# Optimization experiments

Measured on AMD Instinct MI355X. Metric: run time of the kernel, lower is better.

The kernel has to match this reference:

```python
import jax, jax.numpy as jnp
import numpy as np

NUM_HEADS = 16
HEAD_DIM = 64


def setup_inputs() -> dict:
    key = jax.random.key(0)
    ks = jax.random.split(key, 6)
    B, S, E = 4, 1024, 1024
    return {
        "x": jax.random.normal(ks[0], (B, S, E), dtype=jnp.float32),
        "W_qkv": jax.random.normal(ks[1], (E, 3 * E), dtype=jnp.float32) * 0.02,
        "b_qkv": jax.random.normal(ks[2], (3 * E,), dtype=jnp.float32) * 0.02,
        "pe": jax.random.normal(ks[3], (S, S, HEAD_DIM), dtype=jnp.float32) * 0.02,
        "W_out": jax.random.normal(ks[4], (E, E), dtype=jnp.float32) * 0.02,
        "b_out": jax.random.normal(ks[5], (E,), dtype=jnp.float32) * 0.02,
    }


def reference(x, W_qkv, b_qkv, pe, W_out, b_out):
    B, S, E = x.shape
    H, D = NUM_HEADS, HEAD_DIM
    scale = D ** -0.5
    # qkv projection: (B,S,3E) -> (3,B,H,S,D)
    qkv = (x @ W_qkv + b_qkv).reshape(B, S, 3, H, D).transpose(2, 0, 3, 1, 4)
    q, k, v = qkv[0], qkv[1], qkv[2]
    # raw scaled scores (NO softmax in original module)
    scores = jnp.einsum('bhxd,bhyd->bhxy', q, k) * scale
    # relative position bias: pe is (S,S,D) == (x,y,c); original permutes to (c,x,y)
    # then einsum('cxy,bnxc->bnxy', pe, q) -> equivalent to 'xyc,bhxc->bhxy'
    pe_q = jnp.einsum('xyc,bhxc->bhxy', pe, q) * scale
    attn = (scores + pe_q) @ v                      # (B,H,S,D)
    out = attn.transpose(0, 2, 1, 3).reshape(B, S, E)
    return out @ W_out + b_out
```

## Files before the change

kernel.cpp:

```cpp
#include <hip/hip_runtime.h>
#include <cstdint>
#include <cstddef>


typedef unsigned short u16;
typedef unsigned char  u8;
typedef __bf16 bf16x8 __attribute__((ext_vector_type(8)));
typedef float  f32x4  __attribute__((ext_vector_type(4)));
typedef unsigned short u16x8 __attribute__((ext_vector_type(8)));

#define MFMA16(a, b, c) __builtin_amdgcn_mfma_f32_16x16x32_bf16((a), (b), (c), 0, 0, 0)

#define GLOAD16(g, l)                                                        \
    __builtin_amdgcn_global_load_lds(                                        \
        (const __attribute__((address_space(1))) unsigned int*)(g),          \
        (__attribute__((address_space(3))) unsigned int*)(l), 16, 0, 0)

__device__ __forceinline__ u16 f2bf(float f) {
    __bf16 h = (__bf16)f;
    return __builtin_bit_cast(u16, h);
}
__device__ __forceinline__ u16x8 pack8(float4 a, float4 b) {
    u16x8 v;
    v[0] = f2bf(a.x); v[1] = f2bf(a.y); v[2] = f2bf(a.z); v[3] = f2bf(a.w);
    v[4] = f2bf(b.x); v[5] = f2bf(b.y); v[6] = f2bf(b.z); v[7] = f2bf(b.w);
    return v;
}

__device__ __forceinline__ void sbar() {
    asm volatile("" ::: "memory");
    __builtin_amdgcn_s_barrier();
    asm volatile("" ::: "memory");
}
template <int N> __device__ __forceinline__ void waitv() {
    asm volatile("s_waitcnt vmcnt(%0)" :: "n"(N) : "memory");
}

__device__ __forceinline__ void convT_tile(const float* __restrict__ in,
                                           u16* __restrict__ out, int R, int C,
                                           int bx, int by, float (*tile)[68]) {
    const int t  = threadIdx.x;
    const int r0 = by * 64, c0 = bx * 64;
    const int rr = t >> 4, c4 = t & 15;
    for (int p = 0; p < 4; ++p) {
        int r = rr + p * 16;
        float4 v = *(const float4*)&in[(size_t)(r0 + r) * C + c0 + c4 * 4];
        *(float4*)&tile[r][c4 * 4] = v;
    }
    __syncthreads();
    for (int p = 0; p < 4; ++p) {
        int n = rr + p * 16;
        ushort4 o;
        o.x = f2bf(tile[c4 * 4 + 0][n]);
        o.y = f2bf(tile[c4 * 4 + 1][n]);
        o.z = f2bf(tile[c4 * 4 + 2][n]);
        o.w = f2bf(tile[c4 * 4 + 3][n]);
        *(ushort4*)&out[(size_t)(c0 + n) * R + r0 + c4 * 4] = o;
    }
}

__global__ __launch_bounds__(256) void kprep(const float* __restrict__ x,
                                             u16* __restrict__ xb,
                                             const float* __restrict__ Wqkv,
                                             u16* __restrict__ wqkvT,
                                             const float* __restrict__ Wout,
                                             u16* __restrict__ woutT) {
    __shared__ float tile[64][68];
    const int bid = blockIdx.x;
    if (bid < 2048) {
        int i = (bid * 256 + threadIdx.x) * 8;
        float4 f0 = *(const float4*)&x[i];
        float4 f1 = *(const float4*)&x[i + 4];
        *(u16x8*)&xb[i] = pack8(f0, f1);
    } else if (bid < 2816) {
        int r = bid - 2048;
        convT_tile(Wqkv, wqkvT, 1024, 3072, r % 48, r / 48, tile);
    } else {
        int r = bid - 2816;
        convT_tile(Wout, woutT, 1024, 1024, r % 16, r / 16, tile);
    }
}

__global__ __launch_bounds__(256, 2) void kgemm_qkv(const u16* __restrict__ A,
                                                    const u16* __restrict__ WT,
                                                    const float* __restrict__ bias,
                                                    u16* __restrict__ qb,
                                                    u16* __restrict__ kb,
                                                    u16* __restrict__ vtb) {
    __shared__ u16 a_s[128 * 64];
    __shared__ u16 b_s[128 * 64];
    const int t = threadIdx.x;
    const int m0 = blockIdx.y * 128, n0 = blockIdx.x * 128;
    const int lane = t & 63, w = t >> 6, lm = lane & 15, lq = lane >> 4;
    const int mb = (w >> 1) * 64, nb = (w & 1) * 64;
    const int sr = t >> 3, sc = (t & 7) * 8;

    f32x4 acc[4][4] = {};
    for (int k0 = 0; k0 < 1024; k0 += 64) {
        __syncthreads();
#pragma unroll
        for (int p = 0; p < 4; ++p) {
            GLOAD16(&A [(size_t)(m0 + p * 32 + sr) * 1024 + k0 + sc], &a_s[p * 2048 + t * 8]);
            GLOAD16(&WT[(size_t)(n0 + p * 32 + sr) * 1024 + k0 + sc], &b_s[p * 2048 + t * 8]);
        }
        __syncthreads();
#pragma unroll
        for (int ks = 0; ks < 2; ++ks) {
            bf16x8 af[4], bfr[4];
#pragma unroll
            for (int mt = 0; mt < 4; ++mt)
                af[mt] = *(const bf16x8*)&a_s[(mb + mt * 16 + lm) * 64 + ks * 32 + lq * 8];
#pragma unroll
            for (int nt = 0; nt < 4; ++nt)
                bfr[nt] = *(const bf16x8*)&b_s[(nb + nt * 16 + lm) * 64 + ks * 32 + lq * 8];
#pragma unroll
            for (int mt = 0; mt < 4; ++mt)
#pragma unroll
                for (int nt = 0; nt < 4; ++nt)
                    acc[mt][nt] = MFMA16(af[mt], bfr[nt], acc[mt][nt]);
        }
    }
    for (int nt = 0; nt < 4; ++nt) {
        int col = n0 + nb + nt * 16 + lm;
        float bv = bias[col];
        int which = col >> 10;
        int h = (col >> 6) & 15, d = col & 63;
        for (int mt = 0; mt < 4; ++mt) {
            int row0 = m0 + mb + mt * 16 + lq * 4;
            int b = row0 >> 10, s = row0 & 1023;
            if (which == 2) {
                ushort4 o;
                o.x = f2bf(acc[mt][nt][0] + bv);
                o.y = f2bf(acc[mt][nt][1] + bv);
                o.z = f2bf(acc[mt][nt][2] + bv);
                o.w = f2bf(acc[mt][nt][3] + bv);
                *(ushort4*)&vtb[((size_t)(b * 16 + h) * 64 + d) * 1024 + s] = o;
            } else {
                u16* dst = (which == 0) ? qb : kb;
                for (int i = 0; i < 4; ++i)
                    dst[((size_t)((b * 16 + h) * 1024 + s + i)) * 64 + d] =
                        f2bf(acc[mt][nt][i] + bv);
            }
        }
    }
}

__global__ __launch_bounds__(256, 4) void kpq(const u16* __restrict__ qb,
                                              const float* __restrict__ pe,
                                              u8* __restrict__ Pq) {
    __shared__ u16 q_s[64 * 64];
    __shared__ u16 pe_s[2][64 * 80];
    const int x = blockIdx.x;
    const int t = threadIdx.x;
    const int lane = t & 63, w = t >> 6, lm = lane & 15, lq = lane >> 4;
#pragma unroll
    for (int p = 0; p < 2; ++p)
        GLOAD16(&qb[(size_t)((p * 32 + (t >> 3)) * 1024 + x) * 64 + (t & 7) * 8],
                &q_s[p * 2048 + t * 8]);
    const int yl = t >> 2, cq = (t & 3) * 16;
    const float* pex = pe + (size_t)x * 65536;
    float4 r0, r1, r2, r3;
    {
        const float* src = &pex[(size_t)yl * 64 + cq];
        r0 = *(const float4*)&src[0];  r1 = *(const float4*)&src[4];
        r2 = *(const float4*)&src[8];  r3 = *(const float4*)&src[12];
    }
    u8* pq_base = Pq + ((size_t)lm * 1024 + x) * 1024 + lq * 16 + w * 4;
    int cur = 0;
    for (int it = 0; it < 16; ++it) {
        *(u16x8*)&pe_s[cur][yl * 80 + cq]     = pack8(r0, r1);
        *(u16x8*)&pe_s[cur][yl * 80 + cq + 8] = pack8(r2, r3);
        __syncthreads();
        if (it < 15) {
            const float* src = &pex[(size_t)((it + 1) * 64 + yl) * 64 + cq];
            r0 = *(const float4*)&src[0];  r1 = *(const float4*)&src[4];
            r2 = *(const float4*)&src[8];  r3 = *(const float4*)&src[12];
        }
        f32x4 acc[4] = {};
#pragma unroll
        for (int ks = 0; ks < 2; ++ks) {
            bf16x8 a = *(const bf16x8*)&pe_s[cur][(16 * w + lm) * 80 + ks * 32 + lq * 8];
#pragma unroll
            for (int nt = 0; nt < 4; ++nt) {
                bf16x8 b = *(const bf16x8*)&q_s[(nt * 16 + lm) * 64 + ks * 32 + lq * 8];
                acc[nt] = MFMA16(a, b, acc[nt]);
            }
        }
#pragma unroll
        for (int nt = 0; nt < 4; ++nt) {
            unsigned int pw;
            pw = __builtin_amdgcn_cvt_pk_fp8_f32(acc[nt][0], acc[nt][1], 0u, false);
            pw = __builtin_amdgcn_cvt_pk_fp8_f32(acc[nt][2], acc[nt][3], pw, true);
            *(unsigned int*)&pq_base[(size_t)nt * 16 * 1024 * 1024 + it * 64] = pw;
        }
        cur ^= 1;
    }
}

__global__ __launch_bounds__(256, 2) void kattn(const u16* __restrict__ qb,
                                                const u16* __restrict__ kb,
                                                const u16* __restrict__ vt,
                                                const u8* __restrict__ Pq,
                                                u16* __restrict__ attnb) {
    __shared__ u16 q_s[128 * 64];
    __shared__ u16 k_s[2][64 * 64];
    __shared__ u16 v_s[2][64 * 64];
    __shared__ u16 s_s[128 * 80];
    const int bid = blockIdx.x;
    const int bh = bid & 63, x0 = (bid >> 6) * 128;
    const int t = threadIdx.x;
    const int lane = t & 63, w = t >> 6, lm = lane & 15, lq = lane >> 4;
    const int sr = t >> 3, sc = (t & 7) * 8;

#pragma unroll
    for (int p = 0; p < 4; ++p)
        GLOAD16(&qb[(size_t)(bh * 1024 + x0 + p * 32 + sr) * 64 + sc],
                &q_s[p * 2048 + t * 8]);
#pragma unroll
    for (int p = 0; p < 2; ++p) {
        GLOAD16(&kb[(size_t)(bh * 1024 + p * 32 + sr) * 64 + sc],
                &k_s[0][p * 2048 + t * 8]);
        GLOAD16(&vt[(size_t)(bh * 64 + p * 32 + sr) * 1024 + sc],
                &v_s[0][p * 2048 + t * 8]);
    }

    const u8* PqRow = Pq + ((size_t)(bh * 1024) + x0 + 32 * w + lm) * 1024 + lq * 16;
    f32x4 oacc[2][4] = {};

#define ATTN_COMPUTE(CUR, Y0)                                                  \
    {                                                                          \
                 \
        f32x4 sacc[4][2] = {};                                                 \
        _Pragma("unroll")                                                      \
        for (int ks = 0; ks < 2; ++ks) {                                       \
            bf16x8 bq[2];                                                      \
            _Pragma("unroll")                                                  \
            for (int nt = 0; nt < 2; ++nt)                                     \
                bq[nt] = *(const bf16x8*)&q_s[(32 * w + nt * 16 + lm) * 64 + ks * 32 + lq * 8]; \
            _Pragma("unroll")                                                  \
            for (int mt = 0; mt < 4; ++mt) {                                   \
                bf16x8 ak = *(const bf16x8*)&k_s[CUR][(mt * 16 + lm) * 64 + ks * 32 + lq * 8]; \
                _Pragma("unroll")                                              \
                for (int nt = 0; nt < 2; ++nt)                                 \
                    sacc[mt][nt] = MFMA16(ak, bq[nt], sacc[mt][nt]);           \
            }                                                                  \
        }                                                                      \
                \
        _Pragma("unroll")                                                      \
        for (int nt = 0; nt < 2; ++nt) {                                       \
            int xl = 32 * w + nt * 16 + lm;                                    \
            const unsigned int* pqc = (const unsigned int*)&pq4[nt];           \
            _Pragma("unroll")                                                  \
            for (int mt = 0; mt < 4; ++mt) {                                   \
                unsigned int pw = pqc[mt];                                     \
                ushort4 o;                                                     \
                o.x = f2bf((sacc[mt][nt][0] + __builtin_amdgcn_cvt_f32_fp8(pw, 0)) * 0.125f); \
                o.y = f2bf((sacc[mt][nt][1] + __builtin_amdgcn_cvt_f32_fp8(pw, 1)) * 0.125f); \
                o.z = f2bf((sacc[mt][nt][2] + __builtin_amdgcn_cvt_f32_fp8(pw, 2)) * 0.125f); \
                o.w = f2bf((sacc[mt][nt][3] + __builtin_amdgcn_cvt_f32_fp8(pw, 3)) * 0.125f); \
                *(ushort4*)&s_s[xl * 80 + mt * 16 + lq * 4] = o;               \
            }                                                                  \
        }                                                                      \
                                   \
        _Pragma("unroll")                                                      \
        for (int ks = 0; ks < 2; ++ks) {                                       \
            bf16x8 as[2];                                                      \
            _Pragma("unroll")                                                  \
            for (int mt = 0; mt < 2; ++mt)                                     \
                as[mt] = *(const bf16x8*)&s_s[(32 * w + mt * 16 + lm) * 80 + ks * 32 + lq * 8]; \
            _Pragma("unroll")                                                  \
            for (int nt = 0; nt < 4; ++nt) {                                   \
                bf16x8 bv = *(const bf16x8*)&v_s[CUR][(nt * 16 + lm) * 64 + ks * 32 + lq * 8]; \
                _Pragma("unroll")                                              \
                for (int mt = 0; mt < 2; ++mt)                                 \
                    oacc[mt][nt] = MFMA16(as[mt], bv, oacc[mt][nt]);           \
            }                                                                  \
        }                                                                      \
    }

    int cur = 0;
#pragma unroll 1
    for (int it = 0; it < 15; ++it) {
        const int y0 = it * 64;
        sbar();
#pragma unroll
        for (int p = 0; p < 2; ++p) {
            GLOAD16(&kb[(size_t)(bh * 1024 + y0 + 64 + p * 32 + sr) * 64 + sc],
                    &k_s[cur ^ 1][p * 2048 + t * 8]);
            GLOAD16(&vt[(size_t)(bh * 64 + p * 32 + sr) * 1024 + y0 + 64 + sc],
                    &v_s[cur ^ 1][p * 2048 + t * 8]);
        }
        uint4 pq4[2];
#pragma unroll
        for (int nt = 0; nt < 2; ++nt)
            pq4[nt] = *(const uint4*)&PqRow[(size_t)(nt * 16) * 1024 + y0];
        waitv<6>();
        sbar();
        ATTN_COMPUTE(cur, y0)
        cur ^= 1;
    }
    {
        uint4 pq4[2];
#pragma unroll
        for (int nt = 0; nt < 2; ++nt)
            pq4[nt] = *(const uint4*)&PqRow[(size_t)(nt * 16) * 1024 + 960];
        waitv<2>();
        sbar();
        ATTN_COMPUTE(cur, 960)
    }
#undef ATTN_COMPUTE

    const int b = bh >> 4, h = bh & 15;
    for (int mt = 0; mt < 2; ++mt) {
        for (int nt = 0; nt < 4; ++nt) {
            int d = nt * 16 + lm;
            for (int i = 0; i < 4; ++i) {
                int s = x0 + 32 * w + mt * 16 + lq * 4 + i;
                attnb[((size_t)(b * 1024 + s)) * 1024 + h * 64 + d] = f2bf(oacc[mt][nt][i]);
            }
        }
    }
}

__global__ __launch_bounds__(256, 2) void kgemm_out(const u16* __restrict__ A,
                                                    const u16* __restrict__ WT,
                                                    const float* __restrict__ bias,
                                                    float* __restrict__ out) {
    __shared__ u16 a_s[128 * 64];
    __shared__ u16 b_s[128 * 64];
    const int t = threadIdx.x;
    const int m0 = blockIdx.y * 128, n0 = blockIdx.x * 128;
    const int lane = t & 63, w = t >> 6, lm = lane & 15, lq = lane >> 4;
    const int mb = (w >> 1) * 64, nb = (w & 1) * 64;
    const int sr = t >> 3, sc = (t & 7) * 8;

    f32x4 acc[4][4] = {};
    for (int k0 = 0; k0 < 1024; k0 += 64) {
        __syncthreads();
#pragma unroll
        for (int p = 0; p < 4; ++p) {
            GLOAD16(&A [(size_t)(m0 + p * 32 + sr) * 1024 + k0 + sc], &a_s[p * 2048 + t * 8]);
            GLOAD16(&WT[(size_t)(n0 + p * 32 + sr) * 1024 + k0 + sc], &b_s[p * 2048 + t * 8]);
        }
        __syncthreads();
#pragma unroll
        for (int ks = 0; ks < 2; ++ks) {
            bf16x8 af[4], bfr[4];
#pragma unroll
            for (int mt = 0; mt < 4; ++mt)
                af[mt] = *(const bf16x8*)&a_s[(mb + mt * 16 + lm) * 64 + ks * 32 + lq * 8];
#pragma unroll
            for (int nt = 0; nt < 4; ++nt)
                bfr[nt] = *(const bf16x8*)&b_s[(nb + nt * 16 + lm) * 64 + ks * 32 + lq * 8];
#pragma unroll
            for (int mt = 0; mt < 4; ++mt)
#pragma unroll
                for (int nt = 0; nt < 4; ++nt)
                    acc[mt][nt] = MFMA16(af[mt], bfr[nt], acc[mt][nt]);
        }
    }
    for (int nt = 0; nt < 4; ++nt) {
        int col = n0 + nb + nt * 16 + lm;
        float bv = bias[col];
        for (int mt = 0; mt < 4; ++mt) {
            for (int i = 0; i < 4; ++i) {
                int row = m0 + mb + mt * 16 + lq * 4 + i;
                out[(size_t)row * 1024 + col] = acc[mt][nt][i] + bv;
            }
        }
    }
}

extern "C" void kernel_launch(void* const* d_in, const int* in_sizes, int n_in,
                              void* d_out, int out_size, void* d_ws, size_t ws_size,
                              hipStream_t stream) {
    (void)in_sizes; (void)n_in; (void)out_size; (void)ws_size;
    const float* x    = (const float*)d_in[0];
    const float* Wqkv = (const float*)d_in[1];
    const float* bqkv = (const float*)d_in[2];
    const float* pe   = (const float*)d_in[3];
    const float* Wout = (const float*)d_in[4];
    const float* bout = (const float*)d_in[5];
    float* out = (float*)d_out;

    char* ws = (char*)d_ws;
    u16* xb    = (u16*)ws;  ws += (size_t)4096 * 1024 * 2;
    u16* wqkvT = (u16*)ws;  ws += (size_t)3072 * 1024 * 2;
    u16* woutT = (u16*)ws;  ws += (size_t)1024 * 1024 * 2;
    u16* qb    = (u16*)ws;  ws += (size_t)64 * 1024 * 64 * 2;
    u16* kb    = (u16*)ws;  ws += (size_t)64 * 1024 * 64 * 2;
    u16* vtb   = (u16*)ws;  ws += (size_t)64 * 64 * 1024 * 2;
    u16* attnb = (u16*)ws;  ws += (size_t)4 * 1024 * 1024 * 2;
    u8*  pq    = (u8*)ws;   ws += (size_t)64 * 1024 * 1024;

    kprep<<<3072, 256, 0, stream>>>(x, xb, Wqkv, wqkvT, Wout, woutT);
    kgemm_qkv<<<dim3(24, 32), 256, 0, stream>>>(xb, wqkvT, bqkv, qb, kb, vtb);
    kpq<<<1024, 256, 0, stream>>>(qb, pe, pq);
    kattn<<<512, 256, 0, stream>>>(qb, kb, vtb, pq, attnb);
    kgemm_out<<<dim3(8, 32), 256, 0, stream>>>(attnb, woutT, bout, out);
}
```

Measured before the change: 519.9 us.

## Double-buffer LDS tiles in QKV and output GEMM K-loops

Replaces the single-buffered K loop in both projection GEMMs with a shared macro that double-buffers the A and B tiles in LDS. It prefetches the next 64-wide K slice with async global-to-LDS loads while MFMAs run on the current slice, using partial vmcnt waits. This is meant to hide global memory latency behind compute. It doubles LDS use per block to 64KB, which may affect occupancy.

```diff
diff --git a/kernel.cpp b/kernel.cpp
--- a/kernel.cpp
+++ b/kernel.cpp
@@ -81,14 +81,59 @@
     }
 }
 
+#define GEMM_K_LOOP(A_, B_, a_s_, b_s_)                                       \
+    {                                  \
+        _Pragma("unroll")                                                     \
+        for (int p = 0; p < 4; ++p) {                                         \
+            GLOAD16(&A_[(size_t)(m0 + p * 32 + sr) * 1024 + sc],              \
+                    &a_s_[0][p * 2048 + t * 8]);                              \
+            GLOAD16(&B_[(size_t)(n0 + p * 32 + sr) * 1024 + sc],              \
+                    &b_s_[0][p * 2048 + t * 8]);                              \
+        }                                                                     \
+        int cur = 0;                                                          \
+        _Pragma("unroll 1")                                                   \
+        for (int k0 = 0; k0 < 1024; k0 += 64) {                               \
+            if (k0 < 960) {                                                   \
+                sbar();                       \
+                _Pragma("unroll")                                             \
+                for (int p = 0; p < 4; ++p) {                                 \
+                    GLOAD16(&A_[(size_t)(m0 + p * 32 + sr) * 1024 + k0 + 64 + sc], \
+                            &a_s_[cur ^ 1][p * 2048 + t * 8]);                \
+                    GLOAD16(&B_[(size_t)(n0 + p * 32 + sr) * 1024 + k0 + 64 + sc], \
+                            &b_s_[cur ^ 1][p * 2048 + t * 8]);                \
+                }                                                             \
+                waitv<8>();                   \
+            } else {                                                          \
+                waitv<0>();                                                   \
+            }                                                                 \
+            sbar();                          \
+            _Pragma("unroll")                                                 \
+            for (int ks = 0; ks < 2; ++ks) {                                  \
+                bf16x8 af[4], bfr[4];                                         \
+                _Pragma("unroll")                                             \
+                for (int mt = 0; mt < 4; ++mt)                                \
+                    af[mt] = *(const bf16x8*)&a_s_[cur][(mb + mt * 16 + lm) * 64 + ks * 32 + lq * 8]; \
+                _Pragma("unroll")                                             \
+                for (int nt = 0; nt < 4; ++nt)                                \
+                    bfr[nt] = *(const bf16x8*)&b_s_[cur][(nb + nt * 16 + lm) * 64 + ks * 32 + lq * 8]; \
+                _Pragma("unroll")                                             \
+                for (int mt = 0; mt < 4; ++mt)                                \
+                    _Pragma("unroll")                                         \
+                    for (int nt = 0; nt < 4; ++nt)                            \
+                        acc[mt][nt] = MFMA16(af[mt], bfr[nt], acc[mt][nt]);   \
+            }                                                                 \
+            cur ^= 1;                                                         \
+        }                                                                     \
+    }
+
 __global__ __launch_bounds__(256, 2) void kgemm_qkv(const u16* __restrict__ A,
                                                     const u16* __restrict__ WT,
                                                     const float* __restrict__ bias,
                                                     u16* __restrict__ qb,
                                                     u16* __restrict__ kb,
                                                     u16* __restrict__ vtb) {
-    __shared__ u16 a_s[128 * 64];
-    __shared__ u16 b_s[128 * 64];
+    __shared__ u16 a_s[2][128 * 64];
+    __shared__ u16 b_s[2][128 * 64];
     const int t = threadIdx.x;
     const int m0 = blockIdx.y * 128, n0 = blockIdx.x * 128;
     const int lane = t & 63, w = t >> 6, lm = lane & 15, lq = lane >> 4;
@@ -96,30 +141,8 @@
     const int sr = t >> 3, sc = (t & 7) * 8;
 
     f32x4 acc[4][4] = {};
-    for (int k0 = 0; k0 < 1024; k0 += 64) {
-        __syncthreads();
-#pragma unroll
-        for (int p = 0; p < 4; ++p) {
-            GLOAD16(&A [(size_t)(m0 + p * 32 + sr) * 1024 + k0 + sc], &a_s[p * 2048 + t * 8]);
-            GLOAD16(&WT[(size_t)(n0 + p * 32 + sr) * 1024 + k0 + sc], &b_s[p * 2048 + t * 8]);
-        }
-        __syncthreads();
-#pragma unroll
-        for (int ks = 0; ks < 2; ++ks) {
-            bf16x8 af[4], bfr[4];
-#pragma unroll
-            for (int mt = 0; mt < 4; ++mt)
-                af[mt] = *(const bf16x8*)&a_s[(mb + mt * 16 + lm) * 64 + ks * 32 + lq * 8];
-#pragma unroll
-            for (int nt = 0; nt < 4; ++nt)
-                bfr[nt] = *(const bf16x8*)&b_s[(nb + nt * 16 + lm) * 64 + ks * 32 + lq * 8];
-#pragma unroll
-            for (int mt = 0; mt < 4; ++mt)
-#pragma unroll
-                for (int nt = 0; nt < 4; ++nt)
-                    acc[mt][nt] = MFMA16(af[mt], bfr[nt], acc[mt][nt]);
-        }
-    }
+    GEMM_K_LOOP(A, WT, a_s, b_s)
+
     for (int nt = 0; nt < 4; ++nt) {
         int col = n0 + nb + nt * 16 + lm;
         float bv = bias[col];
@@ -326,8 +349,8 @@
                                                     const u16* __restrict__ WT,
                                                     const float* __restrict__ bias,
                                                     float* __restrict__ out) {
-    __shared__ u16 a_s[128 * 64];
-    __shared__ u16 b_s[128 * 64];
+    __shared__ u16 a_s[2][128 * 64];
+    __shared__ u16 b_s[2][128 * 64];
     const int t = threadIdx.x;
     const int m0 = blockIdx.y * 128, n0 = blockIdx.x * 128;
     const int lane = t & 63, w = t >> 6, lm = lane & 15, lq = lane >> 4;
@@ -335,30 +358,8 @@
     const int sr = t >> 3, sc = (t & 7) * 8;
 
     f32x4 acc[4][4] = {};
-    for (int k0 = 0; k0 < 1024; k0 += 64) {
-        __syncthreads();
-#pragma unroll
-        for (int p = 0; p < 4; ++p) {
-            GLOAD16(&A [(size_t)(m0 + p * 32 + sr) * 1024 + k0 + sc], &a_s[p * 2048 + t * 8]);
-            GLOAD16(&WT[(size_t)(n0 + p * 32 + sr) * 1024 + k0 + sc], &b_s[p * 2048 + t * 8]);
-        }
-        __syncthreads();
-#pragma unroll
-        for (int ks = 0; ks < 2; ++ks) {
-            bf16x8 af[4], bfr[4];
-#pragma unroll
-            for (int mt = 0; mt < 4; ++mt)
-                af[mt] = *(const bf16x8*)&a_s[(mb + mt * 16 + lm) * 64 + ks * 32 + lq * 8];
-#pragma unroll
-            for (int nt = 0; nt < 4; ++nt)
-                bfr[nt] = *(const bf16x8*)&b_s[(nb + nt * 16 + lm) * 64 + ks * 32 + lq * 8];
-#pragma unroll
-            for (int mt = 0; mt < 4; ++mt)
-#pragma unroll
-                for (int nt = 0; nt < 4; ++nt)
-                    acc[mt][nt] = MFMA16(af[mt], bfr[nt], acc[mt][nt]);
-        }
-    }
+    GEMM_K_LOOP(A, WT, a_s, b_s)
+
     for (int nt = 0; nt < 4; ++nt) {
         int col = n0 + nb + nt * 16 + lm;
         float bv = bias[col];
```

New measurement: 533.1 us. +2.5%, slower.
